# Optimization experiments

Hardware: AMD Instinct MI355X
Metric: run time of the kernel (lower is better)

## Reference

```python
import jax, jax.numpy as jnp
import numpy as np

N = 100000      # nodes
E = 800000      # edges (avg degree 8)
D_IN = 64
H1 = H2 = H3 = 64
HEADS = 2
D_EDGE = 5
NEG_SLOPE = 0.2  # GATConv leaky_relu slope


def _lin(key, fi, fo):
    kw, kb = jax.random.split(key)
    w = jax.random.normal(kw, (fi, fo), jnp.float32) / np.sqrt(fi)
    b = jax.random.normal(kb, (fo,), jnp.float32) * 0.01
    return w, b


def setup_inputs() -> dict:
    key = jax.random.key(0)
    ks = jax.random.split(key, 16)
    x = jax.random.normal(ks[0], (N, D_IN), jnp.float32)
    edge_index = jax.random.randint(ks[1], (2, E), 0, N, dtype=jnp.int32)
    edge_attr = jax.random.normal(ks[2], (E, D_EDGE), jnp.float32)

    inp = {"x": x, "edge_index": edge_index, "edge_attr": edge_attr}
    dims = [(D_IN, H1), (H1, H2), (H2, H3)]
    for i, (fi, fo) in enumerate(dims, start=1):
        k = jax.random.fold_in(ks[3], i)
        ka, kb, kc = jax.random.split(k, 3)
        inp[f"w_node{i}"], inp[f"b_node{i}"] = _lin(ka, fi, fo)
        inp[f"w_edge{i}"], inp[f"b_edge{i}"] = _lin(kb, D_EDGE, fo)
        inp[f"w_comb{i}"], inp[f"b_comb{i}"] = _lin(kc, 2 * fo, fo)
    # GATConv: shared lin for src/dst, att vectors, bias (concat=False -> size H3)
    kg, ks_, kd, kbias = jax.random.split(ks[4], 4)
    inp["w_gat"] = jax.random.normal(kg, (H3, HEADS * H3), jnp.float32) / np.sqrt(H3)
    inp["att_src"] = jax.random.normal(ks_, (HEADS, H3), jnp.float32) * 0.1
    inp["att_dst"] = jax.random.normal(kd, (HEADS, H3), jnp.float32) * 0.1
    inp["b_gat"] = jax.random.normal(kbias, (H3,), jnp.float32) * 0.01
    return inp


def _edge_conv(h, src, dst, ea, wn, bn, we, be, wc, bc, n):
    # lin_node / lin_edge applied densely, then gather -> concat -> lin -> scatter-add
    hn = h @ wn + bn                       # [N, C]
    ef = ea @ we + be                      # [E, C]
    msg = jnp.concatenate([hn[src], ef], axis=1) @ wc + bc  # [E, C]
    return jax.ops.segment_sum(msg, dst, num_segments=n)


def _gat(h, src, dst, w_gat, att_src, att_dst, b_gat, n):
    g = (h @ w_gat).reshape(n, HEADS, -1)          # [N, H, C]
    a_src = jnp.einsum("nhc,hc->nh", g, att_src)    # [N, H]
    a_dst = jnp.einsum("nhc,hc->nh", g, att_dst)
    alpha = jax.nn.leaky_relu(a_src[src] + a_dst[dst], NEG_SLOPE)  # [E, H]
    # segment softmax over incoming edges of each dst node
    m = jax.ops.segment_max(alpha, dst, num_segments=n)
    alpha = jnp.exp(alpha - m[dst])
    denom = jax.ops.segment_sum(alpha, dst, num_segments=n)
    alpha = alpha / (denom[dst] + 1e-16)
    out = jax.ops.segment_sum(g[src] * alpha[:, :, None], dst, num_segments=n)  # [N,H,C]
    return out.mean(axis=1) + b_gat  # concat=False -> mean over heads, plus bias


def reference(x, edge_index, edge_attr,
              w_node1, b_node1, w_edge1, b_edge1, w_comb1, b_comb1,
              w_node2, b_node2, w_edge2, b_edge2, w_comb2, b_comb2,
              w_node3, b_node3, w_edge3, b_edge3, w_comb3, b_comb3,
              w_gat, att_src, att_dst, b_gat):
    n = x.shape[0]
    src, dst = edge_index[0], edge_index[1]
    h = x
    h = jax.nn.relu(_edge_conv(h, src, dst, edge_attr, w_node1, b_node1, w_edge1, b_edge1, w_comb1, b_comb1, n))
    h = jax.nn.relu(_edge_conv(h, src, dst, edge_attr, w_node2, b_node2, w_edge2, b_edge2, w_comb2, b_comb2, n))
    h = jax.nn.relu(_edge_conv(h, src, dst, edge_attr, w_node3, b_node3, w_edge3, b_edge3, w_comb3, b_comb3, n))
    h = _gat(h, src, dst, w_gat, att_src, att_dst, b_gat, n)
    return h.reshape(-1)  # torch.flatten
```

## Files before the change

kernel.cpp:

```cpp
#include <hip/hip_runtime.h>
#include <hip/hip_fp16.h>
#include <math.h>


#define TPB 256

typedef unsigned int u32;

__device__ inline float2 f16unpack2(u32 u) {
    __half2 h = *reinterpret_cast<__half2*>(&u);
    return __half22float2(h);
}
__device__ inline u32 f16pack2(float lo, float hi) {
    __half2 h = __floats2half2_rn(lo, hi);
    return *reinterpret_cast<u32*>(&h);
}
__device__ inline void fma_f16x8(float* acc, uint4 v, float w) {
    float2 t;
    t = f16unpack2(v.x); acc[0] = fmaf(w, t.x, acc[0]); acc[1] = fmaf(w, t.y, acc[1]);
    t = f16unpack2(v.y); acc[2] = fmaf(w, t.x, acc[2]); acc[3] = fmaf(w, t.y, acc[3]);
    t = f16unpack2(v.z); acc[4] = fmaf(w, t.x, acc[4]); acc[5] = fmaf(w, t.y, acc[5]);
    t = f16unpack2(v.w); acc[6] = fmaf(w, t.x, acc[6]); acc[7] = fmaf(w, t.y, acc[7]);
}
__device__ inline void acc_h16(float4& acc, uint2 v) {
    float2 a = f16unpack2(v.x);
    float2 b = f16unpack2(v.y);
    acc.x += a.x; acc.y += a.y; acc.z += b.x; acc.w += b.y;
}

#define MAC4(acc, a, w0, w1, w2, w3)                                           \
    acc.x = fmaf(a.x, w0.x, acc.x); acc.y = fmaf(a.x, w0.y, acc.y);            \
    acc.z = fmaf(a.x, w0.z, acc.z); acc.w = fmaf(a.x, w0.w, acc.w);            \
    acc.x = fmaf(a.y, w1.x, acc.x); acc.y = fmaf(a.y, w1.y, acc.y);            \
    acc.z = fmaf(a.y, w1.z, acc.z); acc.w = fmaf(a.y, w1.w, acc.w);            \
    acc.x = fmaf(a.z, w2.x, acc.x); acc.y = fmaf(a.z, w2.y, acc.y);            \
    acc.z = fmaf(a.z, w2.z, acc.z); acc.w = fmaf(a.z, w2.w, acc.w);            \
    acc.x = fmaf(a.w, w3.x, acc.x); acc.y = fmaf(a.w, w3.y, acc.y);            \
    acc.z = fmaf(a.w, w3.z, acc.z); acc.w = fmaf(a.w, w3.w, acc.w);

__global__ __launch_bounds__(TPB) void k_hist(const int* __restrict__ dst, int* __restrict__ cnt,
                                              int* __restrict__ rank, int E) {
    int e = blockIdx.x * TPB + threadIdx.x;
    if (e < E) rank[e] = atomicAdd(&cnt[dst[e]], 1);
}

__global__ __launch_bounds__(TPB) void k_scan1(int* __restrict__ data, int* __restrict__ partials, int n) {
    __shared__ int s[TPB];
    int i = blockIdx.x * TPB + threadIdx.x;
    int v = (i < n) ? data[i] : 0;
    s[threadIdx.x] = v;
    __syncthreads();
    for (int off = 1; off < TPB; off <<= 1) {
        int t = (threadIdx.x >= off) ? s[threadIdx.x - off] : 0;
        __syncthreads();
        s[threadIdx.x] += t;
        __syncthreads();
    }
    if (i < n) data[i] = s[threadIdx.x] - v;
    if (threadIdx.x == TPB - 1) partials[blockIdx.x] = s[TPB - 1];
}

__global__ __launch_bounds__(TPB) void k_scan3(int* __restrict__ data, const int* __restrict__ partials,
                                               int n, int total) {
    const int bid = blockIdx.x;
    int s = 0;
    for (int j = threadIdx.x; j < bid; j += TPB) s += partials[j];
    #pragma unroll
    for (int off = 32; off > 0; off >>= 1) s += __shfl_down(s, off);
    __shared__ int ws[4];
    if ((threadIdx.x & 63) == 0) ws[threadIdx.x >> 6] = s;
    __syncthreads();
    int pre = ws[0] + ws[1] + ws[2] + ws[3];
    int i = bid * TPB + threadIdx.x;
    if (i < n) data[i] += pre;
    if (i == 0) data[n] = total;
}

__global__ __launch_bounds__(TPB) void k_scatter(const int* __restrict__ src, const int* __restrict__ dst,
                                                 const int* __restrict__ rank, const int* __restrict__ row_start,
                                                 int2* __restrict__ csr_se, int E) {
    int e = blockIdx.x * TPB + threadIdx.x;
    if (e < E) {
        int idx = row_start[dst[e]] + rank[e];
        csr_se[idx] = make_int2(src[e], e);
    }
}

__global__ __launch_bounds__(TPB) void k_aggB5(const int2* __restrict__ csr_se, const int* __restrict__ row_start,
                                               const float* __restrict__ EA, float* __restrict__ B5, int n) {
    const int node = blockIdx.x * 16 + (threadIdx.x >> 4);
    if (node >= n) return;
    const int lid = threadIdx.x & 15;
    const int beg = row_start[node], end = row_start[node + 1];
    float b0 = 0.f, b1 = 0.f, b2 = 0.f, b3 = 0.f, b4 = 0.f;
    for (int j = beg + lid; j < end; j += 16) {
        int e = csr_se[j].y;
        const float* p = EA + (size_t)e * 5;
        b0 += p[0]; b1 += p[1]; b2 += p[2]; b3 += p[3]; b4 += p[4];
    }
    #pragma unroll
    for (int off = 1; off < 16; off <<= 1) {
        b0 += __shfl_xor(b0, off); b1 += __shfl_xor(b1, off);
        b2 += __shfl_xor(b2, off); b3 += __shfl_xor(b3, off);
        b4 += __shfl_xor(b4, off);
    }
    if (lid == 0) {
        float* bp = B5 + (size_t)node * 5;
        bp[0] = b0; bp[1] = b1; bp[2] = b2; bp[3] = b3; bp[4] = b4;
    }
}

struct CombPtrs {
    const float* wn; const float* bn;
    const float* we; const float* be;
    const float* wc; const float* bc;
    float* W1;
};

__global__ __launch_bounds__(TPB) void k_combine3(CombPtrs p0, CombPtrs p1, CombPtrs p2) {
    CombPtrs P = (blockIdx.x == 0) ? p0 : ((blockIdx.x == 1) ? p1 : p2);
    const float* wn = P.wn; const float* bn = P.bn;
    const float* we = P.we; const float* be = P.be;
    const float* wc = P.wc; const float* bc = P.bc;
    float* W1 = P.W1;
    float* W2 = P.W1 + 4096;
    float* cv = P.W1 + 4416;
    int tid = threadIdx.x;
    for (int idx = tid; idx < 64 * 64; idx += TPB) {
        int i = idx >> 6, j = idx & 63;
        float acc = 0.f;
        #pragma unroll 8
        for (int k = 0; k < 64; k++) acc = fmaf(wn[i * 64 + k], wc[k * 64 + j], acc);
        W1[idx] = acc;
    }
    for (int idx = tid; idx < 5 * 64; idx += TPB) {
        int i = idx >> 6, j = idx & 63;
        float acc = 0.f;
        #pragma unroll 8
        for (int k = 0; k < 64; k++) acc = fmaf(we[i * 64 + k], wc[(64 + k) * 64 + j], acc);
        W2[idx] = acc;
    }
    for (int j = tid; j < 64; j += TPB) {
        float acc = bc[j];
        for (int k = 0; k < 64; k++) {
            acc = fmaf(bn[k], wc[k * 64 + j], acc);
            acc = fmaf(be[k], wc[(64 + k) * 64 + j], acc);
        }
        cv[j] = acc;
    }
}

template <bool IN16, bool OUT16, bool GAT>
__global__ __launch_bounds__(TPB, 4) void k_ec_fused(const void* __restrict__ Hv,
                                                     const int* __restrict__ row_start,
                                                     const int2* __restrict__ csr_se,
                                                     const float* __restrict__ Wfold,
                                                     const float* __restrict__ B5,
                                                     void* __restrict__ OUTv, int n,
                                                     const float* __restrict__ Wg,
                                                     const float* __restrict__ att_src,
                                                     const float* __restrict__ att_dst,
                                                     u32* __restrict__ Gh,
                                                     float* __restrict__ asrc,
                                                     float* __restrict__ adst) {
    __shared__ float Alds[64 * 68];
    const float* Hf = (const float*)Hv;
    const u32*   Hh = (const u32*)Hv;
    const int t = threadIdx.x;
    const int base = blockIdx.x * 64;

    const int lane = t & 63;
    const int lid = lane & 15;
    const int gbase = lane & 48;
    const int gid = t >> 4;
    const int c4 = lid * 4;
    const int h2i = lid * 2;
    for (int i = 0; i < 4; i++) {
        int r = gid * 4 + i;
        int node = base + r;
        float4 acc = make_float4(0.f, 0.f, 0.f, 0.f);
        if (node < n) {
            int beg = row_start[node], end = row_start[node + 1];
            for (int chunk = beg; chunk < end; chunk += 16) {
                int cdeg = min(end - chunk, 16);
                int s_l = (chunk + lid < end) ? csr_se[chunk + lid].x : 0;
                int it = 0;
                for (; it + 7 < cdeg; it += 8) {
                    int se0 = __shfl(s_l, gbase + it);
                    int se1 = __shfl(s_l, gbase + it + 1);
                    int se2 = __shfl(s_l, gbase + it + 2);
                    int se3 = __shfl(s_l, gbase + it + 3);
                    int se4 = __shfl(s_l, gbase + it + 4);
                    int se5 = __shfl(s_l, gbase + it + 5);
                    int se6 = __shfl(s_l, gbase + it + 6);
                    int se7 = __shfl(s_l, gbase + it + 7);
                    if (IN16) {
                        uint2 v0 = *(const uint2*)&Hh[(size_t)se0 * 32 + h2i];
                        uint2 v1 = *(const uint2*)&Hh[(size_t)se1 * 32 + h2i];
                        uint2 v2 = *(const uint2*)&Hh[(size_t)se2 * 32 + h2i];
                        uint2 v3 = *(const uint2*)&Hh[(size_t)se3 * 32 + h2i];
                        uint2 v4 = *(const uint2*)&Hh[(size_t)se4 * 32 + h2i];
                        uint2 v5 = *(const uint2*)&Hh[(size_t)se5 * 32 + h2i];
                        uint2 v6 = *(const uint2*)&Hh[(size_t)se6 * 32 + h2i];
                        uint2 v7 = *(const uint2*)&Hh[(size_t)se7 * 32 + h2i];
                        acc_h16(acc, v0); acc_h16(acc, v1); acc_h16(acc, v2); acc_h16(acc, v3);
                        acc_h16(acc, v4); acc_h16(acc, v5); acc_h16(acc, v6); acc_h16(acc, v7);
                    } else {
                        float4 v0 = *(const float4*)&Hf[(size_t)se0 * 64 + c4];
                        float4 v1 = *(const float4*)&Hf[(size_t)se1 * 64 + c4];
                        float4 v2 = *(const float4*)&Hf[(size_t)se2 * 64 + c4];
                        float4 v3 = *(const float4*)&Hf[(size_t)se3 * 64 + c4];
                        float4 v4 = *(const float4*)&Hf[(size_t)se4 * 64 + c4];
                        float4 v5 = *(const float4*)&Hf[(size_t)se5 * 64 + c4];
                        float4 v6 = *(const float4*)&Hf[(size_t)se6 * 64 + c4];
                        float4 v7 = *(const float4*)&Hf[(size_t)se7 * 64 + c4];
                        acc.x += ((v0.x + v1.x) + (v2.x + v3.x)) + ((v4.x + v5.x) + (v6.x + v7.x));
                        acc.y += ((v0.y + v1.y) + (v2.y + v3.y)) + ((v4.y + v5.y) + (v6.y + v7.y));
                        acc.z += ((v0.z + v1.z) + (v2.z + v3.z)) + ((v4.z + v5.z) + (v6.z + v7.z));
                        acc.w += ((v0.w + v1.w) + (v2.w + v3.w)) + ((v4.w + v5.w) + (v6.w + v7.w));
                    }
                }
                for (; it + 3 < cdeg; it += 4) {
                    int se0 = __shfl(s_l, gbase + it);
                    int se1 = __shfl(s_l, gbase + it + 1);
                    int se2 = __shfl(s_l, gbase + it + 2);
                    int se3 = __shfl(s_l, gbase + it + 3);
                    if (IN16) {
                        uint2 v0 = *(const uint2*)&Hh[(size_t)se0 * 32 + h2i];
                        uint2 v1 = *(const uint2*)&Hh[(size_t)se1 * 32 + h2i];
                        uint2 v2 = *(const uint2*)&Hh[(size_t)se2 * 32 + h2i];
                        uint2 v3 = *(const uint2*)&Hh[(size_t)se3 * 32 + h2i];
                        acc_h16(acc, v0); acc_h16(acc, v1); acc_h16(acc, v2); acc_h16(acc, v3);
                    } else {
                        float4 v0 = *(const float4*)&Hf[(size_t)se0 * 64 + c4];
                        float4 v1 = *(const float4*)&Hf[(size_t)se1 * 64 + c4];
                        float4 v2 = *(const float4*)&Hf[(size_t)se2 * 64 + c4];
                        float4 v3 = *(const float4*)&Hf[(size_t)se3 * 64 + c4];
                        acc.x += (v0.x + v1.x) + (v2.x + v3.x);
                        acc.y += (v0.y + v1.y) + (v2.y + v3.y);
                        acc.z += (v0.z + v1.z) + (v2.z + v3.z);
                        acc.w += (v0.w + v1.w) + (v2.w + v3.w);
                    }
                }
                for (; it < cdeg; it++) {
                    int se = __shfl(s_l, gbase + it);
                    if (IN16) {
                        uint2 v = *(const uint2*)&Hh[(size_t)se * 32 + h2i];
                        acc_h16(acc, v);
                    } else {
                        float4 v = *(const float4*)&Hf[(size_t)se * 64 + c4];
                        acc.x += v.x; acc.y += v.y; acc.z += v.z; acc.w += v.w;
                    }
                }
            }
        }
        *(float4*)&Alds[r * 68 + c4] = acc;
    }
    __syncthreads();

    const int r0 = (t >> 4) * 4, c0 = (t & 15) * 4;
    float4 acc0 = make_float4(0.f, 0.f, 0.f, 0.f), acc1 = acc0, acc2 = acc0, acc3 = acc0;
    #pragma unroll 2
    for (int k = 0; k < 64; k += 4) {
        float4 a0 = *(float4*)&Alds[(r0 + 0) * 68 + k];
        float4 a1 = *(float4*)&Alds[(r0 + 1) * 68 + k];
        float4 a2 = *(float4*)&Alds[(r0 + 2) * 68 + k];
        float4 a3 = *(float4*)&Alds[(r0 + 3) * 68 + k];
        float4 w0 = *(const float4*)&Wfold[(k + 0) * 64 + c0];
        float4 w1 = *(const float4*)&Wfold[(k + 1) * 64 + c0];
        float4 w2 = *(const float4*)&Wfold[(k + 2) * 64 + c0];
        float4 w3 = *(const float4*)&Wfold[(k + 3) * 64 + c0];
        MAC4(acc0, a0, w0, w1, w2, w3);
        MAC4(acc1, a1, w0, w1, w2, w3);
        MAC4(acc2, a2, w0, w1, w2, w3);
        MAC4(acc3, a3, w0, w1, w2, w3);
    }
    float4 w2c[5];
    #pragma unroll
    for (int j = 0; j < 5; j++) w2c[j] = *(const float4*)&Wfold[4096 + j * 64 + c0];
    const float4 cv4 = *(const float4*)&Wfold[4416 + c0];

    if (GAT) __syncthreads();

    #define EC_STORE(i, acc)                                                        \
        { int row = base + r0 + i;                                                  \
          if (row < n) {                                                            \
              const float* bp = B5 + (size_t)row * 5;                               \
              float deg = (float)(row_start[row + 1] - row_start[row]);             \
              float4 q;                                                             \
              q.x = deg * cv4.x; q.y = deg * cv4.y;                                 \
              q.z = deg * cv4.z; q.w = deg * cv4.w;                                 \
              for (int j = 0; j < 5; j++) {                                         \
                  float b = bp[j];                                                  \
                  q.x = fmaf(b, w2c[j].x, q.x); q.y = fmaf(b, w2c[j].y, q.y);       \
                  q.z = fmaf(b, w2c[j].z, q.z); q.w = fmaf(b, w2c[j].w, q.w);       \
              }                                                                     \
              float4 r4;                                                            \
              r4.x = fmaxf(acc.x + q.x, 0.f); r4.y = fmaxf(acc.y + q.y, 0.f);       \
              r4.z = fmaxf(acc.z + q.z, 0.f); r4.w = fmaxf(acc.w + q.w, 0.f);       \
              if (GAT) {                                                            \
                  *(float4*)&Alds[(r0 + i) * 68 + c0] = r4;                         \
              } else if (OUT16) {                                                   \
                  u32* O = (u32*)OUTv;                                              \
                  uint2 gg;                                                         \
                  gg.x = f16pack2(r4.x, r4.y); gg.y = f16pack2(r4.z, r4.w);         \
                  *(uint2*)&O[(size_t)row * 32 + (c0 >> 1)] = gg;                   \
              } else {                                                              \
                  float* O = (float*)OUTv;                                          \
                  *(float4*)&O[(size_t)row * 64 + c0] = r4;                         \
              } } }
    EC_STORE(0, acc0) EC_STORE(1, acc1) EC_STORE(2, acc2) EC_STORE(3, acc3)
    #undef EC_STORE

    if (GAT) {
        __syncthreads();
        float4 p00 = make_float4(0.f, 0.f, 0.f, 0.f), p01 = p00, p02 = p00, p03 = p00;
        float4 p10 = p00, p11 = p00, p12 = p00, p13 = p00;
        #pragma unroll 2
        for (int k = 0; k < 64; k += 4) {
            float4 a0 = *(float4*)&Alds[(r0 + 0) * 68 + k];
            float4 a1 = *(float4*)&Alds[(r0 + 1) * 68 + k];
            float4 a2 = *(float4*)&Alds[(r0 + 2) * 68 + k];
            float4 a3 = *(float4*)&Alds[(r0 + 3) * 68 + k];
            float4 u0 = *(const float4*)&Wg[(k + 0) * 128 + c0];
            float4 u1 = *(const float4*)&Wg[(k + 1) * 128 + c0];
            float4 u2 = *(const float4*)&Wg[(k + 2) * 128 + c0];
            float4 u3 = *(const float4*)&Wg[(k + 3) * 128 + c0];
            MAC4(p00, a0, u0, u1, u2, u3);
            MAC4(p01, a1, u0, u1, u2, u3);
            MAC4(p02, a2, u0, u1, u2, u3);
            MAC4(p03, a3, u0, u1, u2, u3);
            float4 v0 = *(const float4*)&Wg[(k + 0) * 128 + 64 + c0];
            float4 v1 = *(const float4*)&Wg[(k + 1) * 128 + 64 + c0];
            float4 v2 = *(const float4*)&Wg[(k + 2) * 128 + 64 + c0];
            float4 v3 = *(const float4*)&Wg[(k + 3) * 128 + 64 + c0];
            MAC4(p10, a0, v0, v1, v2, v3);
            MAC4(p11, a1, v0, v1, v2, v3);
            MAC4(p12, a2, v0, v1, v2, v3);
            MAC4(p13, a3, v0, v1, v2, v3);
        }
        const float4 as0 = *(const float4*)&att_src[c0];
        const float4 as1 = *(const float4*)&att_src[64 + c0];
        const float4 ad0 = *(const float4*)&att_dst[c0];
        const float4 ad1 = *(const float4*)&att_dst[64 + c0];
        #define DOT4(a, b) (a.x * b.x + a.y * b.y + a.z * b.z + a.w * b.w)
        #define GAT_ROW(i, h0, h1)                                                      \
            { int row = base + r0 + i;                                                  \
              float s0 = DOT4(h0, as0), s1 = DOT4(h1, as1);                             \
              float d0 = DOT4(h0, ad0), d1 = DOT4(h1, ad1);                             \
              s0 += __shfl_xor(s0, 1); s1 += __shfl_xor(s1, 1);                         \
              d0 += __shfl_xor(d0, 1); d1 += __shfl_xor(d1, 1);                         \
              s0 += __shfl_xor(s0, 2); s1 += __shfl_xor(s1, 2);                         \
              d0 += __shfl_xor(d0, 2); d1 += __shfl_xor(d1, 2);                         \
              s0 += __shfl_xor(s0, 4); s1 += __shfl_xor(s1, 4);                         \
              d0 += __shfl_xor(d0, 4); d1 += __shfl_xor(d1, 4);                         \
              s0 += __shfl_xor(s0, 8); s1 += __shfl_xor(s1, 8);                         \
              d0 += __shfl_xor(d0, 8); d1 += __shfl_xor(d1, 8);                         \
              if (row < n) {                                                            \
                  uint2 g0; g0.x = f16pack2(h0.x, h0.y); g0.y = f16pack2(h0.z, h0.w);   \
                  uint2 g1; g1.x = f16pack2(h1.x, h1.y); g1.y = f16pack2(h1.z, h1.w);   \
                  *(uint2*)&Gh[(size_t)row * 64 + (c0 >> 1)] = g0;                      \
                  *(uint2*)&Gh[(size_t)row * 64 + 32 + (c0 >> 1)] = g1;                 \
                  if ((t & 15) == 0) {                                                  \
                      float2 sv; sv.x = s0; sv.y = s1;                                  \
                      float2 dv; dv.x = d0; dv.y = d1;                                  \
                      *(float2*)&asrc[(size_t)row * 2] = sv;                            \
                      *(float2*)&adst[(size_t)row * 2] = dv; } } }
        GAT_ROW(0, p00, p10) GAT_ROW(1, p01, p11) GAT_ROW(2, p02, p12) GAT_ROW(3, p03, p13)
        #undef GAT_ROW
        #undef DOT4
    }
}

__global__ __launch_bounds__(TPB) void k_gat_agg(const u32* __restrict__ Gh, const int* __restrict__ row_start,
                                                 const int2* __restrict__ csr_se, const float* __restrict__ asrc,
                                                 const float* __restrict__ adst, const float* __restrict__ bgat,
                                                 float* __restrict__ OUT, int n) {
    const int node = blockIdx.x * 16 + (threadIdx.x >> 4);
    if (node >= n) return;
    const int lane = threadIdx.x & 63;
    const int lid = lane & 15;
    const int gbase = lane & 48;
    const int head = lid >> 3;
    const int u4 = lid * 4;
    const int beg = row_start[node], end = row_start[node + 1];
    const float2 adv = *(const float2*)&adst[(size_t)node * 2];
    float m0 = -INFINITY, m1 = -INFINITY, d0 = 0.f, d1 = 0.f;
    float A[8] = {0.f, 0.f, 0.f, 0.f, 0.f, 0.f, 0.f, 0.f};
    for (int chunk = beg; chunk < end; chunk += 16) {
        int cdeg = min(end - chunk, 16);
        bool valid = (lid < cdeg);
        int s_l = valid ? csr_se[chunk + lid].x : 0;
        float al0 = -INFINITY, al1 = -INFINITY;
        if (valid) {
            float2 av = *(const float2*)&asrc[(size_t)s_l * 2];
            float t0 = av.x + adv.x, t1 = av.y + adv.y;
            al0 = (t0 > 0.f) ? t0 : 0.2f * t0;
            al1 = (t1 > 0.f) ? t1 : 0.2f * t1;
        }
        float cm0 = al0, cm1 = al1;
        #pragma unroll
        for (int off = 1; off < 16; off <<= 1) {
            cm0 = fmaxf(cm0, __shfl_xor(cm0, off));
            cm1 = fmaxf(cm1, __shfl_xor(cm1, off));
        }
        float nm0 = fmaxf(m0, cm0), nm1 = fmaxf(m1, cm1);
        float sc0 = __expf(m0 - nm0), sc1 = __expf(m1 - nm1);
        float w0 = valid ? __expf(al0 - nm0) : 0.f;
        float w1 = valid ? __expf(al1 - nm1) : 0.f;
        float cd0 = w0, cd1 = w1;
        #pragma unroll
        for (int off = 1; off < 16; off <<= 1) {
            cd0 += __shfl_xor(cd0, off);
            cd1 += __shfl_xor(cd1, off);
        }
        d0 = d0 * sc0 + cd0;
        d1 = d1 * sc1 + cd1;
        float scsel = head ? sc1 : sc0;
        #pragma unroll
        for (int j = 0; j < 8; j++) A[j] *= scsel;
        m0 = nm0; m1 = nm1;
        int it = 0;
        for (; it + 3 < cdeg; it += 4) {
            int sa = __shfl(s_l, gbase + it);
            int sb = __shfl(s_l, gbase + it + 1);
            int sc = __shfl(s_l, gbase + it + 2);
            int sd = __shfl(s_l, gbase + it + 3);
            float w0a = __shfl(w0, gbase + it),     w1a = __shfl(w1, gbase + it);
            float w0b = __shfl(w0, gbase + it + 1), w1b = __shfl(w1, gbase + it + 1);
            float w0c = __shfl(w0, gbase + it + 2), w1c = __shfl(w1, gbase + it + 2);
            float w0d = __shfl(w0, gbase + it + 3), w1d = __shfl(w1, gbase + it + 3);
            float wa = head ? w1a : w0a;
            float wb = head ? w1b : w0b;
            float wc = head ? w1c : w0c;
            float wd = head ? w1d : w0d;
            uint4 va = *(const uint4*)&Gh[(size_t)sa * 64 + u4];
            uint4 vb = *(const uint4*)&Gh[(size_t)sb * 64 + u4];
            uint4 vc = *(const uint4*)&Gh[(size_t)sc * 64 + u4];
            uint4 vd = *(const uint4*)&Gh[(size_t)sd * 64 + u4];
            fma_f16x8(A, va, wa);
            fma_f16x8(A, vb, wb);
            fma_f16x8(A, vc, wc);
            fma_f16x8(A, vd, wd);
        }
        for (; it + 1 < cdeg; it += 2) {
            int sa = __shfl(s_l, gbase + it);
            int sb = __shfl(s_l, gbase + it + 1);
            float w0a = __shfl(w0, gbase + it),     w1a = __shfl(w1, gbase + it);
            float w0b = __shfl(w0, gbase + it + 1), w1b = __shfl(w1, gbase + it + 1);
            float wa = head ? w1a : w0a;
            float wb = head ? w1b : w0b;
            uint4 va = *(const uint4*)&Gh[(size_t)sa * 64 + u4];
            uint4 vb = *(const uint4*)&Gh[(size_t)sb * 64 + u4];
            fma_f16x8(A, va, wa);
            fma_f16x8(A, vb, wb);
        }
        if (it < cdeg) {
            int sa = __shfl(s_l, gbase + it);
            float w0a = __shfl(w0, gbase + it), w1a = __shfl(w1, gbase + it);
            float wa = head ? w1a : w0a;
            uint4 va = *(const uint4*)&Gh[(size_t)sa * 64 + u4];
            fma_f16x8(A, va, wa);
        }
    }
    float rh = 0.5f / ((head ? d1 : d0) + 1e-16f);
    #pragma unroll
    for (int j = 0; j < 8; j++) {
        A[j] *= rh;
        A[j] += __shfl_xor(A[j], 8);
    }
    if (head == 0) {
        int cb = (lid & 7) * 8;
        const float4 bg0 = *(const float4*)&bgat[cb];
        const float4 bg1 = *(const float4*)&bgat[cb + 4];
        float4 o0; o0.x = A[0] + bg0.x; o0.y = A[1] + bg0.y; o0.z = A[2] + bg0.z; o0.w = A[3] + bg0.w;
        float4 o1; o1.x = A[4] + bg1.x; o1.y = A[5] + bg1.y; o1.z = A[6] + bg1.z; o1.w = A[7] + bg1.w;
        float* op = &OUT[(size_t)node * 64 + cb];
        *(float4*)op = o0;
        *(float4*)(op + 4) = o1;
    }
}

extern "C" void kernel_launch(void* const* d_in, const int* in_sizes, int n_in,
                              void* d_out, int out_size, void* d_ws, size_t ws_size,
                              hipStream_t stream) {
    const float* x   = (const float*)d_in[0];
    const int*   ei  = (const int*)d_in[1];
    const float* ea  = (const float*)d_in[2];
    const int N = in_sizes[0] / 64;
    const int E = in_sizes[1] / 2;
    const int* src = ei;
    const int* dst = ei + E;

    const float* wn[3] = {(const float*)d_in[3],  (const float*)d_in[9],  (const float*)d_in[15]};
    const float* bn[3] = {(const float*)d_in[4],  (const float*)d_in[10], (const float*)d_in[16]};
    const float* we[3] = {(const float*)d_in[5],  (const float*)d_in[11], (const float*)d_in[17]};
    const float* be[3] = {(const float*)d_in[6],  (const float*)d_in[12], (const float*)d_in[18]};
    const float* wc[3] = {(const float*)d_in[7],  (const float*)d_in[13], (const float*)d_in[19]};
    const float* bc[3] = {(const float*)d_in[8],  (const float*)d_in[14], (const float*)d_in[20]};
    const float* wgat    = (const float*)d_in[21];
    const float* att_src = (const float*)d_in[22];
    const float* att_dst = (const float*)d_in[23];
    const float* bgat    = (const float*)d_in[24];

    char* ws = (char*)d_ws;
    size_t off = 0;
    auto alloc = [&](size_t bytes) -> void* {
        void* p = ws + off;
        off = (off + bytes + 255) & ~(size_t)255;
        return p;
    };
    int*   row_start = (int*)alloc((size_t)(N + 1) * 4);
    int*   partials  = (int*)alloc(1024 * 4);
    int*   rank      = (int*)alloc((size_t)E * 4);
    int2*  csr_se    = (int2*)alloc((size_t)E * 8);
    float* Wc        = (float*)alloc((size_t)3 * 4480 * 4);
    float* B5        = (float*)alloc((size_t)N * 5 * 4);
    u32*   bufH0     = (u32*)alloc((size_t)N * 64 * 2);
    u32*   bufH1     = (u32*)alloc((size_t)N * 64 * 2);
    u32*   Gh        = (u32*)alloc((size_t)N * 64 * 4);
    float* asrc      = (float*)alloc((size_t)N * 2 * 4);
    float* adst      = (float*)alloc((size_t)N * 2 * 4);
    float* out = (float*)d_out;

    const int nbN = (N + TPB - 1) / TPB;
    const int nbE = (E + TPB - 1) / TPB;
    const int grpBlocks = (N + 15) / 16;
    const int tiles = (N + 63) / 64;

    CombPtrs p0 = {wn[0], bn[0], we[0], be[0], wc[0], bc[0], Wc};
    CombPtrs p1 = {wn[1], bn[1], we[1], be[1], wc[1], bc[1], Wc + 4480};
    CombPtrs p2 = {wn[2], bn[2], we[2], be[2], wc[2], bc[2], Wc + 2 * 4480};
    k_combine3<<<3, TPB, 0, stream>>>(p0, p1, p2);

    hipMemsetAsync(row_start, 0, (size_t)N * 4, stream);
    k_hist<<<nbE, TPB, 0, stream>>>(dst, row_start, rank, E);
    k_scan1<<<nbN, TPB, 0, stream>>>(row_start, partials, N);
    k_scan3<<<nbN, TPB, 0, stream>>>(row_start, partials, N, E);
    k_scatter<<<nbE, TPB, 0, stream>>>(src, dst, rank, row_start, csr_se, E);
    k_aggB5<<<grpBlocks, TPB, 0, stream>>>(csr_se, row_start, ea, B5, N);

    k_ec_fused<false, true, false><<<tiles, TPB, 0, stream>>>(
        x,     row_start, csr_se, Wc,            B5, bufH0, N,
        nullptr, nullptr, nullptr, nullptr, nullptr, nullptr);
    k_ec_fused<true,  true, false><<<tiles, TPB, 0, stream>>>(
        bufH0, row_start, csr_se, Wc + 4480,     B5, bufH1, N,
        nullptr, nullptr, nullptr, nullptr, nullptr, nullptr);
    k_ec_fused<true,  true, true><<<tiles, TPB, 0, stream>>>(
        bufH1, row_start, csr_se, Wc + 2 * 4480, B5, nullptr, N,
        wgat, att_src, att_dst, Gh, asrc, adst);

    k_gat_agg<<<grpBlocks, TPB, 0, stream>>>(Gh, row_start, csr_se, asrc, adst, bgat, out, N);
}
```

Measured before the change: 415.8 us.

## Convert input features and GAT weights to fp16, stage GAT weights in LDS

Adds a pre-pass that converts the fp32 node features to fp16 so the first edge-conv layer gathers half-width rows like the later layers do. The GAT projection weights are also converted to fp16 in an extra block of the combine kernel and loaded into shared memory, instead of being read as fp32 from global memory inside the inner loop. The launch-bounds occupancy hint is raised from 4 to 6. The cost is an extra conversion kernel and more fp16 rounding on the inputs and GAT weights, and the 16KB of added LDS in the GAT variant may limit its occupancy.

```diff
diff --git a/kernel.cpp b/kernel.cpp
--- a/kernel.cpp
+++ b/kernel.cpp
@@ -10,6 +10,10 @@
 __device__ inline float2 f16unpack2(u32 u) {
     __half2 h = *reinterpret_cast<__half2*>(&u);
     return __half22float2(h);
+}
+__device__ inline float4 f16unpack4(uint2 q) {
+    float2 a = f16unpack2(q.x), b = f16unpack2(q.y);
+    return make_float4(a.x, a.y, b.x, b.y);
 }
 __device__ inline u32 f16pack2(float lo, float hi) {
     __half2 h = __floats2half2_rn(lo, hi);
@@ -37,6 +41,17 @@
     acc.z = fmaf(a.z, w2.z, acc.z); acc.w = fmaf(a.z, w2.w, acc.w);            \
     acc.x = fmaf(a.w, w3.x, acc.x); acc.y = fmaf(a.w, w3.y, acc.y);            \
     acc.z = fmaf(a.w, w3.z, acc.z); acc.w = fmaf(a.w, w3.w, acc.w);
+
+__global__ __launch_bounds__(TPB) void k_cvt16(const float4* __restrict__ X, uint4* __restrict__ XH, int n8) {
+    int i = blockIdx.x * TPB + threadIdx.x;
+    if (i < n8) {
+        float4 a = X[i * 2], b = X[i * 2 + 1];
+        uint4 o;
+        o.x = f16pack2(a.x, a.y); o.y = f16pack2(a.z, a.w);
+        o.z = f16pack2(b.x, b.y); o.w = f16pack2(b.z, b.w);
+        XH[i] = o;
+    }
+}
 
 __global__ __launch_bounds__(TPB) void k_hist(const int* __restrict__ dst, int* __restrict__ cnt,
                                               int* __restrict__ rank, int E) {
@@ -117,7 +132,15 @@
     float* W1;
 };
 
-__global__ __launch_bounds__(TPB) void k_combine3(CombPtrs p0, CombPtrs p1, CombPtrs p2) {
+__global__ __launch_bounds__(TPB) void k_combine4(CombPtrs p0, CombPtrs p1, CombPtrs p2,
+                                                  const float* __restrict__ wg, u32* __restrict__ wgh) {
+    if (blockIdx.x == 3) {
+        for (int i = threadIdx.x; i < 4096; i += TPB) {
+            float2 v = *(const float2*)&wg[i * 2];
+            wgh[i] = f16pack2(v.x, v.y);
+        }
+        return;
+    }
     CombPtrs P = (blockIdx.x == 0) ? p0 : ((blockIdx.x == 1) ? p1 : p2);
     const float* wn = P.wn; const float* bn = P.bn;
     const float* we = P.we; const float* be = P.be;
@@ -151,23 +174,32 @@
 }
 
 template <bool IN16, bool OUT16, bool GAT>
-__global__ __launch_bounds__(TPB, 4) void k_ec_fused(const void* __restrict__ Hv,
+__global__ __launch_bounds__(TPB, 6) void k_ec_fused(const void* __restrict__ Hv,
                                                      const int* __restrict__ row_start,
                                                      const int2* __restrict__ csr_se,
                                                      const float* __restrict__ Wfold,
                                                      const float* __restrict__ B5,
                                                      void* __restrict__ OUTv, int n,
-                                                     const float* __restrict__ Wg,
+                                                     const u32* __restrict__ Wgh,
                                                      const float* __restrict__ att_src,
                                                      const float* __restrict__ att_dst,
                                                      u32* __restrict__ Gh,
                                                      float* __restrict__ asrc,
                                                      float* __restrict__ adst) {
     __shared__ float Alds[64 * 68];
+    __shared__ u32 Wglds[GAT ? 4096 : 4];
     const float* Hf = (const float*)Hv;
     const u32*   Hh = (const u32*)Hv;
     const int t = threadIdx.x;
     const int base = blockIdx.x * 64;
+
+    if (GAT) {
+        #pragma unroll
+        for (int rep = 0; rep < 4; rep++) {
+            int i = rep * 256 + t;
+            *(uint4*)&Wglds[i * 4] = ((const uint4*)Wgh)[i];
+        }
+    }
 
     const int lane = t & 63;
     const int lid = lane & 15;
@@ -322,18 +354,18 @@
             float4 a1 = *(float4*)&Alds[(r0 + 1) * 68 + k];
             float4 a2 = *(float4*)&Alds[(r0 + 2) * 68 + k];
             float4 a3 = *(float4*)&Alds[(r0 + 3) * 68 + k];
-            float4 u0 = *(const float4*)&Wg[(k + 0) * 128 + c0];
-            float4 u1 = *(const float4*)&Wg[(k + 1) * 128 + c0];
-            float4 u2 = *(const float4*)&Wg[(k + 2) * 128 + c0];
-            float4 u3 = *(const float4*)&Wg[(k + 3) * 128 + c0];
+            float4 u0 = f16unpack4(*(uint2*)&Wglds[(k + 0) * 64 + (c0 >> 1)]);
+            float4 u1 = f16unpack4(*(uint2*)&Wglds[(k + 1) * 64 + (c0 >> 1)]);
+            float4 u2 = f16unpack4(*(uint2*)&Wglds[(k + 2) * 64 + (c0 >> 1)]);
+            float4 u3 = f16unpack4(*(uint2*)&Wglds[(k + 3) * 64 + (c0 >> 1)]);
             MAC4(p00, a0, u0, u1, u2, u3);
             MAC4(p01, a1, u0, u1, u2, u3);
             MAC4(p02, a2, u0, u1, u2, u3);
             MAC4(p03, a3, u0, u1, u2, u3);
-            float4 v0 = *(const float4*)&Wg[(k + 0) * 128 + 64 + c0];
-            float4 v1 = *(const float4*)&Wg[(k + 1) * 128 + 64 + c0];
-            float4 v2 = *(const float4*)&Wg[(k + 2) * 128 + 64 + c0];
-            float4 v3 = *(const float4*)&Wg[(k + 3) * 128 + 64 + c0];
+            float4 v0 = f16unpack4(*(uint2*)&Wglds[(k + 0) * 64 + 32 + (c0 >> 1)]);
+            float4 v1 = f16unpack4(*(uint2*)&Wglds[(k + 1) * 64 + 32 + (c0 >> 1)]);
+            float4 v2 = f16unpack4(*(uint2*)&Wglds[(k + 2) * 64 + 32 + (c0 >> 1)]);
+            float4 v3 = f16unpack4(*(uint2*)&Wglds[(k + 3) * 64 + 32 + (c0 >> 1)]);
             MAC4(p10, a0, v0, v1, v2, v3);
             MAC4(p11, a1, v0, v1, v2, v3);
             MAC4(p12, a2, v0, v1, v2, v3);
@@ -515,7 +547,9 @@
     int*   rank      = (int*)alloc((size_t)E * 4);
     int2*  csr_se    = (int2*)alloc((size_t)E * 8);
     float* Wc        = (float*)alloc((size_t)3 * 4480 * 4);
+    u32*   Wgh       = (u32*)alloc((size_t)4096 * 4);
     float* B5        = (float*)alloc((size_t)N * 5 * 4);
+    u32*   xh        = (u32*)alloc((size_t)N * 64 * 2);
     u32*   bufH0     = (u32*)alloc((size_t)N * 64 * 2);
     u32*   bufH1     = (u32*)alloc((size_t)N * 64 * 2);
     u32*   Gh        = (u32*)alloc((size_t)N * 64 * 4);
@@ -527,11 +561,15 @@
     const int nbE = (E + TPB - 1) / TPB;
     const int grpBlocks = (N + 15) / 16;
     const int tiles = (N + 63) / 64;
+    const int n8 = N * 8;
+    const int nbC = (n8 + TPB - 1) / TPB;
 
     CombPtrs p0 = {wn[0], bn[0], we[0], be[0], wc[0], bc[0], Wc};
     CombPtrs p1 = {wn[1], bn[1], we[1], be[1], wc[1], bc[1], Wc + 4480};
     CombPtrs p2 = {wn[2], bn[2], we[2], be[2], wc[2], bc[2], Wc + 2 * 4480};
-    k_combine3<<<3, TPB, 0, stream>>>(p0, p1, p2);
+    k_combine4<<<4, TPB, 0, stream>>>(p0, p1, p2, wgat, Wgh);
+
+    k_cvt16<<<nbC, TPB, 0, stream>>>((const float4*)x, (uint4*)xh, n8);
 
     hipMemsetAsync(row_start, 0, (size_t)N * 4, stream);
     k_hist<<<nbE, TPB, 0, stream>>>(dst, row_start, rank, E);
@@ -540,15 +578,15 @@
     k_scatter<<<nbE, TPB, 0, stream>>>(src, dst, rank, row_start, csr_se, E);
     k_aggB5<<<grpBlocks, TPB, 0, stream>>>(csr_se, row_start, ea, B5, N);
 
-    k_ec_fused<false, true, false><<<tiles, TPB, 0, stream>>>(
-        x,     row_start, csr_se, Wc,            B5, bufH0, N,
+    k_ec_fused<true, true, false><<<tiles, TPB, 0, stream>>>(
+        xh,    row_start, csr_se, Wc,            B5, bufH0, N,
         nullptr, nullptr, nullptr, nullptr, nullptr, nullptr);
-    k_ec_fused<true,  true, false><<<tiles, TPB, 0, stream>>>(
+    k_ec_fused<true, true, false><<<tiles, TPB, 0, stream>>>(
         bufH0, row_start, csr_se, Wc + 4480,     B5, bufH1, N,
         nullptr, nullptr, nullptr, nullptr, nullptr, nullptr);
-    k_ec_fused<true,  true, true><<<tiles, TPB, 0, stream>>>(
+    k_ec_fused<true, true, true><<<tiles, TPB, 0, stream>>>(
         bufH1, row_start, csr_se, Wc + 2 * 4480, B5, nullptr, N,
-        wgat, att_src, att_dst, Gh, asrc, adst);
+        Wgh, att_src, att_dst, Gh, asrc, adst);
 
     k_gat_agg<<<grpBlocks, TPB, 0, stream>>>(Gh, row_start, csr_se, asrc, adst, bgat, out, N);
 }
```

After: 409.2 us. Within noise of the previous version (-1.6%).
